# Performance work log

Hardware: AMD Instinct MI355X
Metric: run time of the kernel (lower is better)

Reference implementation:

```python
import jax, jax.numpy as jnp
import numpy as np

B, NPTS = 32, 2048          # batch, raw points per cloud
G, M = 128, 32              # num_group (FPS centers), group_size (KNN)
C, DEPTH, H = 384, 12, 8    # trans_dim, depth, num_heads
HD = C // H                 # head_dim = 48, divisible by 6 for 3-axis RoPE
MLP = 4 * C
CLS = 40
THETA = 100.0


def _ln(x, g, b):
    m = x.mean(-1, keepdims=True)
    v = ((x - m) ** 2).mean(-1, keepdims=True)
    return (x - m) * jax.lax.rsqrt(v + 1e-5) * g + b


def _rot_pairs(x, cos, sin):
    # rotate consecutive (even, odd) pairs of the last dim by angle arrays
    x2 = x.reshape(x.shape[:-1] + (-1, 2))
    xr, xi = x2[..., 0], x2[..., 1]
    return jnp.stack([xr * cos - xi * sin, xr * sin + xi * cos], -1).reshape(x.shape)


def _fps(pts, n):
    # farthest point sampling, first point = index 0
    Bb, N, _ = pts.shape

    def step(carry, _):
        dist, last = carry
        lp = jnp.take_along_axis(pts, last[:, None, None], axis=1)  # (B,1,3)
        dist = jnp.minimum(dist, jnp.sum((pts - lp) ** 2, -1))
        nxt = jnp.argmax(dist, -1).astype(jnp.int32)
        return (dist, nxt), last

    init = (jnp.full((Bb, N), 1e10, pts.dtype), jnp.zeros((Bb,), jnp.int32))
    _, idxs = jax.lax.scan(step, init, None, length=n)
    return idxs.T  # (B, n)


def forward(pts, enc_w1, enc_b1, enc_g1, enc_be1, enc_w2, enc_b2,
            enc_w3, enc_b3, enc_g2, enc_be2, enc_w4, enc_b4,
            cls_token, cls_pos,
            ln1_g, ln1_b, qkv_w, givens_theta, proj_w, proj_b,
            ln2_g, ln2_b, fc1_w, fc1_b, fc2_w, fc2_b,
            norm_g, norm_b,
            hw1, hb1, hg1, hbe1, hw2, hb2, hg2, hbe2, hw3, hb3):
    # ---- Group divider: FPS centers + KNN neighborhoods ----
    cidx = _fps(pts, G)
    center = jnp.take_along_axis(pts, cidx[:, :, None], axis=1)          # (B,G,3)
    d2 = jnp.sum((center[:, :, None, :] - pts[:, None, :, :]) ** 2, -1)  # (B,G,N)
    _, kidx = jax.lax.top_k(-d2, M)                                      # (B,G,M)
    neigh = jax.vmap(lambda p, i: p[i])(pts, kidx) - center[:, :, None, :]

    # ---- mini-PointNet encoder (BN in eval mode: running mean 0, var 1) ----
    x = neigh.reshape(B * G, M, 3)
    f = jax.nn.relu((x @ enc_w1.T + enc_b1) * enc_g1 + enc_be1)          # (BG,M,128)
    f = f @ enc_w2.T + enc_b2                                            # (BG,M,256)
    fg = jnp.max(f, 1, keepdims=True)
    f = jnp.concatenate([jnp.broadcast_to(fg, f.shape), f], -1)          # (BG,M,512)
    f = jax.nn.relu((f @ enc_w3.T + enc_b3) * enc_g2 + enc_be2)
    f = f @ enc_w4.T + enc_b4                                            # (BG,M,C)
    tok = jnp.max(f, 1).reshape(B, G, C)

    # ---- 3-axis axial RoPE frequencies from group centers ----
    nfr = HD // 6
    fr = 1.0 / (THETA ** (jnp.arange(nfr, dtype=pts.dtype) * 2.0 / (HD // 3)))
    ang = (center[..., None] * fr).reshape(B, G, 3 * nfr)                # (B,G,HD/2)
    pcos, psin = jnp.cos(ang)[:, None], jnp.sin(ang)[:, None]            # (B,1,G,HD/2)

    # ---- tokens: [CLS | groups] ----
    x = jnp.concatenate([jnp.broadcast_to(cls_token + cls_pos, (B, 1, C)), tok], 1)
    N = G + 1
    scale = HD ** -0.5

    for i in range(DEPTH):
        h = _ln(x, ln1_g[i], ln1_b[i])
        qkv = (h @ qkv_w[i].T).reshape(B, N, 3, H, HD).transpose(2, 0, 3, 1, 4)
        q, k, v = qkv[0], qkv[1], qkv[2]                                 # (B,H,N,HD)
        # learnable Givens rotation (per-head block-diagonal pair rotations)
        gcos = jnp.cos(givens_theta[i])[None, :, None]                   # (1,H,1,HD/2)
        gsin = jnp.sin(givens_theta[i])[None, :, None]
        q = _rot_pairs(q, gcos, gsin)
        k = _rot_pairs(k, gcos, gsin)
        # positional RoPE on non-CLS tokens only
        q = jnp.concatenate([q[:, :, :1], _rot_pairs(q[:, :, 1:], pcos, psin)], 2)
        k = jnp.concatenate([k[:, :, :1], _rot_pairs(k[:, :, 1:], pcos, psin)], 2)
        attn = jax.nn.softmax(jnp.einsum('bhqd,bhkd->bhqk', q, k) * scale, -1)
        o = jnp.einsum('bhqk,bhkd->bhqd', attn, v).transpose(0, 2, 1, 3).reshape(B, N, C)
        x = x + o @ proj_w[i].T + proj_b[i]
        h = _ln(x, ln2_g[i], ln2_b[i])
        x = x + jax.nn.gelu(h @ fc1_w[i].T + fc1_b[i], approximate=False) @ fc2_w[i].T + fc2_b[i]

    x = _ln(x, norm_g, norm_b)
    feat = jnp.concatenate([x[:, 0], jnp.max(x[:, 1:], 1)], -1)          # (B,2C)
    hfe = jax.nn.relu((feat @ hw1.T + hb1) * hg1 + hbe1)
    hfe = jax.nn.relu((hfe @ hw2.T + hb2) * hg2 + hbe2)
    return hfe @ hw3.T + hb3                                             # (B,CLS)


def setup_inputs() -> dict:
    key = jax.random.key(0)
    ks = iter(jax.random.split(key, 64))
    nrm = lambda *s: jax.random.normal(next(ks), s, jnp.float32) * 0.02
    d = dict(
        pts=jax.random.normal(next(ks), (B, NPTS, 3), jnp.float32),
        enc_w1=nrm(128, 3), enc_b1=jnp.zeros(128), enc_g1=jnp.ones(128), enc_be1=jnp.zeros(128),
        enc_w2=nrm(256, 128), enc_b2=jnp.zeros(256),
        enc_w3=nrm(512, 512), enc_b3=jnp.zeros(512), enc_g2=jnp.ones(512), enc_be2=jnp.zeros(512),
        enc_w4=nrm(C, 512), enc_b4=jnp.zeros(C),
        cls_token=nrm(1, 1, C), cls_pos=nrm(1, 1, C),
        ln1_g=jnp.ones((DEPTH, C)), ln1_b=jnp.zeros((DEPTH, C)),
        qkv_w=nrm(DEPTH, 3 * C, C), givens_theta=nrm(DEPTH, H, HD // 2),
        proj_w=nrm(DEPTH, C, C), proj_b=jnp.zeros((DEPTH, C)),
        ln2_g=jnp.ones((DEPTH, C)), ln2_b=jnp.zeros((DEPTH, C)),
        fc1_w=nrm(DEPTH, MLP, C), fc1_b=jnp.zeros((DEPTH, MLP)),
        fc2_w=nrm(DEPTH, C, MLP), fc2_b=jnp.zeros((DEPTH, C)),
        norm_g=jnp.ones(C), norm_b=jnp.zeros(C),
        hw1=nrm(256, 2 * C), hb1=jnp.zeros(256), hg1=jnp.ones(256), hbe1=jnp.zeros(256),
        hw2=nrm(256, 256), hb2=jnp.zeros(256), hg2=jnp.ones(256), hbe2=jnp.zeros(256),
        hw3=nrm(CLS, 256), hb3=jnp.zeros(CLS),
    )
    return d


def reference(pts, enc_w1, enc_b1, enc_g1, enc_be1, enc_w2, enc_b2,
              enc_w3, enc_b3, enc_g2, enc_be2, enc_w4, enc_b4,
              cls_token, cls_pos,
              ln1_g, ln1_b, qkv_w, givens_theta, proj_w, proj_b,
              ln2_g, ln2_b, fc1_w, fc1_b, fc2_w, fc2_b,
              norm_g, norm_b,
              hw1, hb1, hg1, hbe1, hw2, hb2, hg2, hbe2, hw3, hb3):
    return forward(pts, enc_w1, enc_b1, enc_g1, enc_be1, enc_w2, enc_b2,
                   enc_w3, enc_b3, enc_g2, enc_be2, enc_w4, enc_b4,
                   cls_token, cls_pos,
                   ln1_g, ln1_b, qkv_w, givens_theta, proj_w, proj_b,
                   ln2_g, ln2_b, fc1_w, fc1_b, fc2_w, fc2_b,
                   norm_g, norm_b,
                   hw1, hb1, hg1, hbe1, hw2, hb2, hg2, hbe2, hw3, hb3)
```

## Files before the change

### kernel.cpp

```cpp
#include <hip/hip_runtime.h>
#include <math.h>

constexpr int kB   = 32;
constexpr int kN   = 2048;
constexpr int kG   = 128;
constexpr int kM   = 32;
constexpr int kC   = 384;
constexpr int kH   = 8;
constexpr int kHD  = 48;
constexpr int kNT  = 129;
constexpr int kMLP = 1536;
constexpr int kRows = kB * kNT;
constexpr int kGC  = 512;
constexpr int kRC  = kGC * kM;

typedef __attribute__((ext_vector_type(8))) short bf16x8;
typedef __attribute__((ext_vector_type(4))) float f32x4;

__device__ __forceinline__ unsigned short f2bf(float x) {
  unsigned u = __float_as_uint(x);
  unsigned r = (u + 0x7fffu + ((u >> 16) & 1u)) >> 16;
  return (unsigned short)r;
}
__device__ __forceinline__ float bf2f(unsigned short u) {
  return __uint_as_float(((unsigned)u) << 16);
}

__global__ __launch_bounds__(128, 1) void fps_kernel(
    const float* __restrict__ pts, float* __restrict__ center)
{
  #pragma clang fp contract(off)
  __shared__ float sx[kN + 64], sy[kN + 64], sz[kN + 64];
  __shared__ float rvv[2];
  __shared__ int   rii[2];
  const int b = blockIdx.x, t = threadIdx.x;
  const int lane = t & 63, w = t >> 6;
  const float* P = pts + (size_t)b * kN * 3;
  float rx[16], ry[16], rz[16], rd[16];
  const int base = t * 16;
  #pragma unroll
  for (int j = 0; j < 16; ++j) {
    int i = base + j;
    float x = P[3*i], y = P[3*i+1], z = P[3*i+2];
    rx[j] = x; ry[j] = y; rz[j] = z; rd[j] = 1e10f;
    int ii = i + (i >> 5);
    sx[ii] = x; sy[ii] = y; sz[ii] = z;
  }
  __syncthreads();
  int last = 0;
  float* cb = center + (size_t)b * kG * 3;
  for (int it = 0; it < kG; ++it) {
    int ls = last + (last >> 5);
    float lx = sx[ls], ly = sy[ls], lz = sz[ls];
    if (t == 0) { cb[3*it] = lx; cb[3*it+1] = ly; cb[3*it+2] = lz; }
    float bestv = -1.0f; int besti = kN;
    #pragma unroll
    for (int j = 0; j < 16; ++j) {
      float dx = rx[j]-lx, dy = ry[j]-ly, dz = rz[j]-lz;
      float d = (dx*dx + dy*dy) + dz*dz;
      float nd = fminf(rd[j], d);
      rd[j] = nd;
      if (nd > bestv) { bestv = nd; besti = base + j; }
    }
    #pragma unroll
    for (int off = 1; off < 64; off <<= 1) {
      float vv = __shfl_xor(bestv, off);
      int   ii = __shfl_xor(besti, off);
      if (vv > bestv || (vv == bestv && ii < besti)) { bestv = vv; besti = ii; }
    }
    if (lane == 0) { rvv[w] = bestv; rii[w] = besti; }
    __syncthreads();
    float v0 = rvv[0], v1 = rvv[1];
    int   i0 = rii[0], i1 = rii[1];
    last = (v1 > v0) ? i1 : i0;
    __syncthreads();
  }
}

__global__ void rope_kernel(const float* __restrict__ center,
                            float* __restrict__ pcs, float* __restrict__ psn)
{
  int idx = blockIdx.x*256 + threadIdx.x;
  if (idx >= kB*kG*24) return;
  int p  = idx % 24;
  int bg = idx / 24;
  int axis = p >> 3, j = p & 7;
  float e  = (float)(2*j) / 16.0f;
  float fr = 1.0f / powf(100.0f, e);
  float ang = center[(size_t)bg*3 + axis] * fr;
  pcs[idx] = cosf(ang);
  psn[idx] = sinf(ang);
}

__global__ __launch_bounds__(256) void knn_kernel(
    const float* __restrict__ pts, const float* __restrict__ center,
    float* __restrict__ neigh)
{
  #pragma clang fp contract(off)
  __shared__ float sx[kN + kN/32], sy[kN + kN/32], sz[kN + kN/32];
  const int t = threadIdx.x;
  const int lane = t & 63, w = t >> 6;
  const int blk = blockIdx.x;
  const int b = blk >> 5;
  const float* P = pts + (size_t)b * kN * 3;
  for (int i = t; i < kN; i += 256) {
    int ii = i + (i >> 5);
    sx[ii] = P[3*i]; sy[ii] = P[3*i+1]; sz[ii] = P[3*i+2];
  }
  __syncthreads();
  const int bg = b*kG + (blk & 31)*4 + w;
  const float cx = center[(size_t)bg*3+0];
  const float cy = center[(size_t)bg*3+1];
  const float cz = center[(size_t)bg*3+2];
  float rd[32];
  const int base = lane * 32;
  #pragma unroll
  for (int j = 0; j < 32; ++j) {
    int is = lane*33 + j;
    float dx = cx - sx[is], dy = cy - sy[is], dz = cz - sz[is];
    rd[j] = (dx*dx + dy*dy) + dz*dz;
  }
  float* ob = neigh + (size_t)bg * kM * 3;
  int lastWin = -1;
  for (int m = 0; m < kM; ++m) {
    float bestv = 3.0e38f; int besti = kN;
    #pragma unroll
    for (int j = 0; j < 32; ++j) {
      float v = rd[j];
      if (base + j == lastWin) v = 3.0e38f;
      rd[j] = v;
      if (v < bestv) { bestv = v; besti = base + j; }
    }
    #pragma unroll
    for (int off = 1; off < 64; off <<= 1) {
      float vv = __shfl_xor(bestv, off);
      int   i2 = __shfl_xor(besti, off);
      if (vv < bestv || (vv == bestv && i2 < besti)) { bestv = vv; besti = i2; }
    }
    lastWin = besti;
    if (lane == 0) {
      int is = besti + (besti >> 5);
      ob[3*m+0] = sx[is] - cx; ob[3*m+1] = sy[is] - cy; ob[3*m+2] = sz[is] - cz;
    }
  }
}

__global__ void wcvt_kernel(const float* __restrict__ s,
                            unsigned short* __restrict__ d, int n)
{
  int i = (blockIdx.x*256 + threadIdx.x)*8;
  if (i >= n) return;
  float4 a = *(const float4*)(s + i), b = *(const float4*)(s + i + 4);
  bf16x8 v;
  v[0]=(short)f2bf(a.x); v[1]=(short)f2bf(a.y); v[2]=(short)f2bf(a.z); v[3]=(short)f2bf(a.w);
  v[4]=(short)f2bf(b.x); v[5]=(short)f2bf(b.y); v[6]=(short)f2bf(b.z); v[7]=(short)f2bf(b.w);
  *(bf16x8*)(d + i) = v;
}

__global__ void wcvt4_kernel(const float* __restrict__ q, const float* __restrict__ p,
                             const float* __restrict__ f1, const float* __restrict__ f2,
                             unsigned short* __restrict__ d)
{
  int i = (blockIdx.x*256 + threadIdx.x)*8;
  const float* s; int lo;
  if (i < 442368)       { s = q;  lo = i; }
  else if (i < 589824)  { s = p;  lo = i - 442368; }
  else if (i < 1179648) { s = f1; lo = i - 589824; }
  else                  { s = f2; lo = i - 1179648; }
  float4 a = *(const float4*)(s + lo), b = *(const float4*)(s + lo + 4);
  bf16x8 v;
  v[0]=(short)f2bf(a.x); v[1]=(short)f2bf(a.y); v[2]=(short)f2bf(a.z); v[3]=(short)f2bf(a.w);
  v[4]=(short)f2bf(b.x); v[5]=(short)f2bf(b.y); v[6]=(short)f2bf(b.z); v[7]=(short)f2bf(b.w);
  *(bf16x8*)(d + i) = v;
}

__global__ __launch_bounds__(256) void enc1_kernel(
    const float* __restrict__ neighC,
    const float* __restrict__ w1, const float* __restrict__ b1,
    const float* __restrict__ g1, const float* __restrict__ be1,
    unsigned short* __restrict__ f1c)
{
  const int t = threadIdx.x;
  const int r = blockIdx.x*2 + (t >> 7);
  const int c = t & 127;
  const float* nr = neighC + (size_t)r*3;
  float x0 = nr[0], x1 = nr[1], x2 = nr[2];
  float s = x0*w1[3*c] + x1*w1[3*c+1] + x2*w1[3*c+2] + b1[c];
  float v = fmaxf(s*g1[c] + be1[c], 0.0f);
  f1c[(size_t)r*128 + c] = f2bf(v);
}

__global__ __launch_bounds__(256) void pool2_kernel(
    const unsigned short* __restrict__ f2c, unsigned short* __restrict__ fgc)
{
  const int g = blockIdx.x, c = threadIdx.x;
  float mx = -3.0e38f;
  #pragma unroll 8
  for (int m = 0; m < kM; ++m)
    mx = fmaxf(mx, bf2f(f2c[((size_t)g*kM + m)*256 + c]));
  fgc[(size_t)g*256 + c] = f2bf(mx);
}

template <int EPI, int FM, int FN>
__global__ __launch_bounds__(256) void mgemm_kernel(
    const unsigned short* __restrict__ A, int lda,
    const unsigned short* __restrict__ Bb, int ldb,
    void* __restrict__ Cv,
    const float* __restrict__ bias,
    const float* __restrict__ aux,
    const float* __restrict__ gsc, const float* __restrict__ bsc,
    int Mm, int Nn, int Kk,
    float* __restrict__ poolOut, int poolG0)
{
  constexpr int BM = FM*32, BN = FN*32;
  __shared__ unsigned short As[BM][72];
  __shared__ unsigned short Bs[BN][72];
  const int t = threadIdx.x;
  const int m0 = blockIdx.x * BM;
  const int n0 = blockIdx.y * BN;
  const int w = t >> 6, lane = t & 63;
  const int wm = w >> 1, wn = w & 1;
  const int lr = lane & 15;
  const int lk = (lane >> 4) * 8;
  const int srow = t >> 3;
  const int skseg = (t & 7) * 8;
  f32x4 acc[FM][FN] = {};
  for (int k0 = 0; k0 < Kk; k0 += 64) {
    #pragma unroll
    for (int p = 0; p < BM/32; ++p) {
      int r = p*32 + srow;
      int gr = m0 + r;
      bf16x8 av = {};
      if (gr < Mm) av = *(const bf16x8*)(A + (size_t)gr*lda + k0 + skseg);
      *(bf16x8*)(&As[r][skseg]) = av;
    }
    #pragma unroll
    for (int p = 0; p < BN/32; ++p) {
      int r = p*32 + srow;
      bf16x8 bv = *(const bf16x8*)(Bb + (size_t)(n0 + r)*ldb + k0 + skseg);
      *(bf16x8*)(&Bs[r][skseg]) = bv;
    }
    __syncthreads();
    #pragma unroll
    for (int kk = 0; kk < 64; kk += 32) {
      bf16x8 af[FM], bf[FN];
      #pragma unroll
      for (int i = 0; i < FM; ++i)
        af[i] = *(const bf16x8*)(&As[wm*(FM*16) + i*16 + lr][kk + lk]);
      #pragma unroll
      for (int i = 0; i < FN; ++i)
        bf[i] = *(const bf16x8*)(&Bs[wn*(FN*16) + i*16 + lr][kk + lk]);
      #pragma unroll
      for (int i = 0; i < FM; ++i)
        #pragma unroll
        for (int j = 0; j < FN; ++j)
          acc[i][j] = __builtin_amdgcn_mfma_f32_16x16x32_bf16(af[i], bf[j], acc[i][j], 0, 0, 0);
    }
    __syncthreads();
  }

  if constexpr (EPI == 4) {
    #pragma unroll
    for (int ni = 0; ni < FN; ++ni) {
      int cc = n0 + wn*(FN*16) + ni*16 + lr;
      float mx = -3.0e38f;
      #pragma unroll
      for (int mi = 0; mi < FM; ++mi)
        #pragma unroll
        for (int j = 0; j < 4; ++j)
          mx = fmaxf(mx, acc[mi][ni][j]);
      mx = fmaxf(mx, __shfl_xor(mx, 16));
      mx = fmaxf(mx, __shfl_xor(mx, 32));
      if ((lane >> 4) == 0) {
        int ggl = poolG0 + (m0 >> 5) + wm;
        int b = ggl >> 7, g = ggl & 127;
        poolOut[((size_t)b*kNT + 1 + g)*kC + cc] = mx + bias[cc];
      }
    }
    return;
  }

  #pragma unroll
  for (int mi = 0; mi < FM; ++mi) {
    #pragma unroll
    for (int j = 0; j < 4; ++j) {
      int r = m0 + wm*(FM*16) + mi*16 + (lane >> 4)*4 + j;
      if (r < Mm) {
        #pragma unroll
        for (int ni = 0; ni < FN; ++ni) {
          int cc = n0 + wn*(FN*16) + ni*16 + lr;
          float v = acc[mi][ni][j];
          size_t o = (size_t)r*Nn + cc;
          if constexpr (EPI == 0) {
            ((unsigned short*)Cv)[o] = f2bf(v);
          } else if constexpr (EPI == 1) {
            ((unsigned short*)Cv)[o] = f2bf(v + bias[cc]);
          } else if constexpr (EPI == 2) {
            ((float*)Cv)[o] = v + bias[cc];
          } else if constexpr (EPI == 3) {
            float u = (v + aux[(size_t)(r >> 5)*Nn + cc])*gsc[cc] + bsc[cc];
            ((unsigned short*)Cv)[o] = f2bf(fmaxf(u, 0.0f));
          } else if constexpr (EPI == 5) {
            ((float*)Cv)[o] = aux[o] + v + bias[cc];
          } else {
            float u = v + bias[cc];
            ((unsigned short*)Cv)[o] = f2bf(0.5f*u*(1.0f + erff(u*0.70710678118654752440f)));
          }
        }
      }
    }
  }
}

__global__ void cls_kernel(const float* __restrict__ ct, const float* __restrict__ cp,
                           float* __restrict__ x)
{
  int idx = blockIdx.x*256 + threadIdx.x;
  if (idx >= kB*kC) return;
  int b = idx / kC, c = idx % kC;
  x[(size_t)b*kNT*kC + c] = ct[c] + cp[c];
}

template <int OUTBF>
__global__ __launch_bounds__(256) void ln_kernel(
    const float* __restrict__ in, void* __restrict__ outv,
    const float* __restrict__ g, const float* __restrict__ bb)
{
  const int t = threadIdx.x;
  const int lane = t & 63;
  const int row = blockIdx.x*4 + (t >> 6);
  const float* p = in + (size_t)row*kC;
  float v[6];
  #pragma unroll
  for (int k = 0; k < 6; ++k) v[k] = p[k*64 + lane];
  float s = 0.f;
  #pragma unroll
  for (int k = 0; k < 6; ++k) s += v[k];
  #pragma unroll
  for (int off = 1; off < 64; off <<= 1) s += __shfl_xor(s, off);
  float mean = s / 384.0f;
  float vs = 0.f;
  #pragma unroll
  for (int k = 0; k < 6; ++k) { float d = v[k]-mean; vs += d*d; }
  #pragma unroll
  for (int off = 1; off < 64; off <<= 1) vs += __shfl_xor(vs, off);
  float r = rsqrtf(vs / 384.0f + 1e-5f);
  #pragma unroll
  for (int k = 0; k < 6; ++k) {
    int c = k*64 + lane;
    float o = (v[k]-mean)*r*g[c] + bb[c];
    if constexpr (OUTBF) ((unsigned short*)outv)[(size_t)row*kC + c] = f2bf(o);
    else                 ((float*)outv)[(size_t)row*kC + c] = o;
  }
}

__global__ __launch_bounds__(512) void attn_kernel(
    const unsigned short* __restrict__ qkv, const float* __restrict__ pcs,
    const float* __restrict__ psn, const float* __restrict__ gth,
    unsigned short* __restrict__ o)
{
  __shared__ float qs[kNT][kHD];
  __shared__ float ks[kNT][52];
  __shared__ float vt[kHD][132];
  __shared__ float gcs[24], gss[24];
  __shared__ float ps[8][132];
  const int t = threadIdx.x;
  const int bh = blockIdx.x;
  const int b = bh >> 3, hh = bh & 7;
  if (t < 24) { float th = gth[hh*24 + t]; gcs[t] = cosf(th); gss[t] = sinf(th); }
  __syncthreads();
  for (int idx = t; idx < kNT*24; idx += 512) {
    int n = idx / 24, p = idx % 24;
    const unsigned short* base = qkv + ((size_t)(b*kNT + n))*1152 + hh*kHD + 2*p;
    float q0 = bf2f(base[0]),   q1 = bf2f(base[1]);
    float k0 = bf2f(base[384]), k1 = bf2f(base[385]);
    float v0 = bf2f(base[768]), v1 = bf2f(base[769]);
    float cg = gcs[p], sg = gss[p];
    float qr = q0*cg - q1*sg, qi = q0*sg + q1*cg;
    float kr = k0*cg - k1*sg, ki = k0*sg + k1*cg;
    if (n > 0) {
      size_t pi = ((size_t)b*kG + (n-1))*24 + p;
      float pc = pcs[pi], pv = psn[pi];
      float tq = qr*pc - qi*pv; qi = qr*pv + qi*pc; qr = tq;
      float tk = kr*pc - ki*pv; ki = kr*pv + ki*pc; kr = tk;
    }
    qs[n][2*p] = qr; qs[n][2*p+1] = qi;
    ks[n][2*p] = kr; ks[n][2*p+1] = ki;
    vt[2*p][n] = v0; vt[2*p+1][n] = v1;
  }
  __syncthreads();
  const int lane = t & 63, w = t >> 6;
  for (int r = w; r < kNT; r += 8) {
    float4 q[12];
    #pragma unroll
    for (int d = 0; d < 12; ++d) q[d] = *(const float4*)(&qs[r][d*4]);
    float sv[3];
    float mx = -3.0e38f;
    #pragma unroll
    for (int ji = 0; ji < 3; ++ji) {
      int j = ji*64 + lane;
      float s = -3.0e38f;
      if (j < kNT) {
        float a0 = 0.f, a1 = 0.f;
        #pragma unroll
        for (int d = 0; d < 12; d += 2) {
          float4 k0v = *(const float4*)(&ks[j][d*4]);
          float4 k1v = *(const float4*)(&ks[j][d*4+4]);
          a0 += q[d].x*k0v.x + q[d].y*k0v.y + q[d].z*k0v.z + q[d].w*k0v.w;
          a1 += q[d+1].x*k1v.x + q[d+1].y*k1v.y + q[d+1].z*k1v.z + q[d+1].w*k1v.w;
        }
        s = (a0 + a1) * 0.14433756729740643f;
      }
      sv[ji] = s;
      mx = fmaxf(mx, s);
    }
    #pragma unroll
    for (int off = 1; off < 64; off <<= 1) mx = fmaxf(mx, __shfl_xor(mx, off));
    float sum = 0.f;
    #pragma unroll
    for (int ji = 0; ji < 3; ++ji) {
      int j = ji*64 + lane;
      if (j < kNT) { float e = expf(sv[ji] - mx); ps[w][j] = e; sum += e; }
    }
    #pragma unroll
    for (int off = 1; off < 64; off <<= 1) sum += __shfl_xor(sum, off);
    if (lane < kHD) {
      float ac0 = 0.f, ac1 = 0.f, ac2 = 0.f, ac3 = 0.f;
      for (int j4 = 0; j4 < 128; j4 += 16) {
        float4 p0 = *(const float4*)(&ps[w][j4]);
        float4 p1 = *(const float4*)(&ps[w][j4+4]);
        float4 p2 = *(const float4*)(&ps[w][j4+8]);
        float4 p3 = *(const float4*)(&ps[w][j4+12]);
        float4 v0 = *(const float4*)(&vt[lane][j4]);
        float4 v1 = *(const float4*)(&vt[lane][j4+4]);
        float4 v2 = *(const float4*)(&vt[lane][j4+8]);
        float4 v3 = *(const float4*)(&vt[lane][j4+12]);
        ac0 += p0.x*v0.x + p0.y*v0.y + p0.z*v0.z + p0.w*v0.w;
        ac1 += p1.x*v1.x + p1.y*v1.y + p1.z*v1.z + p1.w*v1.w;
        ac2 += p2.x*v2.x + p2.y*v2.y + p2.z*v2.z + p2.w*v2.w;
        ac3 += p3.x*v3.x + p3.y*v3.y + p3.z*v3.z + p3.w*v3.w;
      }
      float accv = ((ac0 + ac1) + (ac2 + ac3)) + ps[w][128]*vt[lane][128];
      o[((size_t)(b*kNT + r))*kC + hh*kHD + lane] = f2bf(accv / sum);
    }
  }
}

__global__ __launch_bounds__(256) void head_kernel(
    const float* __restrict__ xf,
    const float* __restrict__ hw1, const float* __restrict__ hb1,
    const float* __restrict__ hg1, const float* __restrict__ hbe1,
    const float* __restrict__ hw2, const float* __restrict__ hb2,
    const float* __restrict__ hg2, const float* __restrict__ hbe2,
    const float* __restrict__ hw3, const float* __restrict__ hb3,
    float* __restrict__ out)
{
  __shared__ float f[768];
  __shared__ float h1[256], h2[256];
  const int t = threadIdx.x;
  const int b = blockIdx.x;
  const float* xb = xf + (size_t)b*kNT*kC;
  for (int c = t; c < kC; c += 256) {
    f[c] = xb[c];
    float mx = -3.0e38f;
    for (int n = 1; n < kNT; ++n) mx = fmaxf(mx, xb[(size_t)n*kC + c]);
    f[kC + c] = mx;
  }
  __syncthreads();
  {
    float acc = hb1[t];
    for (int k = 0; k < 768; k += 4) {
      float4 wv = *(const float4*)(hw1 + (size_t)t*768 + k);
      float4 fv = *(const float4*)(&f[k]);
      acc += fv.x*wv.x + fv.y*wv.y + fv.z*wv.z + fv.w*wv.w;
    }
    h1[t] = fmaxf(acc*hg1[t] + hbe1[t], 0.0f);
  }
  __syncthreads();
  {
    float acc = hb2[t];
    for (int k = 0; k < 256; k += 4) {
      float4 wv = *(const float4*)(hw2 + (size_t)t*256 + k);
      float4 fv = *(const float4*)(&h1[k]);
      acc += fv.x*wv.x + fv.y*wv.y + fv.z*wv.z + fv.w*wv.w;
    }
    h2[t] = fmaxf(acc*hg2[t] + hbe2[t], 0.0f);
  }
  __syncthreads();
  if (t < 40) {
    float acc = hb3[t];
    for (int k = 0; k < 256; k += 4) {
      float4 wv = *(const float4*)(hw3 + (size_t)t*256 + k);
      float4 fv = *(const float4*)(&h2[k]);
      acc += fv.x*wv.x + fv.y*wv.y + fv.z*wv.z + fv.w*wv.w;
    }
    out[(size_t)b*40 + t] = acc;
  }
}

extern "C" void kernel_launch(void* const* d_in, const int* in_sizes, int n_in,
                              void* d_out, int out_size, void* d_ws, size_t ws_size,
                              hipStream_t stream) {
  const float* pts     = (const float*)d_in[0];
  const float* enc_w1  = (const float*)d_in[1];
  const float* enc_b1  = (const float*)d_in[2];
  const float* enc_g1  = (const float*)d_in[3];
  const float* enc_be1 = (const float*)d_in[4];
  const float* enc_w2  = (const float*)d_in[5];
  const float* enc_b2  = (const float*)d_in[6];
  const float* enc_w3  = (const float*)d_in[7];
  const float* enc_b3  = (const float*)d_in[8];
  const float* enc_g2  = (const float*)d_in[9];
  const float* enc_be2 = (const float*)d_in[10];
  const float* enc_w4  = (const float*)d_in[11];
  const float* enc_b4  = (const float*)d_in[12];
  const float* cls_tok = (const float*)d_in[13];
  const float* cls_pos = (const float*)d_in[14];
  const float* ln1_g   = (const float*)d_in[15];
  const float* ln1_b   = (const float*)d_in[16];
  const float* qkv_w   = (const float*)d_in[17];
  const float* givens  = (const float*)d_in[18];
  const float* proj_w  = (const float*)d_in[19];
  const float* proj_b  = (const float*)d_in[20];
  const float* ln2_g   = (const float*)d_in[21];
  const float* ln2_b   = (const float*)d_in[22];
  const float* fc1_w   = (const float*)d_in[23];
  const float* fc1_b   = (const float*)d_in[24];
  const float* fc2_w   = (const float*)d_in[25];
  const float* fc2_b   = (const float*)d_in[26];
  const float* norm_g  = (const float*)d_in[27];
  const float* norm_b  = (const float*)d_in[28];
  const float* hw1     = (const float*)d_in[29];
  const float* hb1     = (const float*)d_in[30];
  const float* hg1     = (const float*)d_in[31];
  const float* hbe1    = (const float*)d_in[32];
  const float* hw2     = (const float*)d_in[33];
  const float* hb2     = (const float*)d_in[34];
  const float* hg2     = (const float*)d_in[35];
  const float* hbe2    = (const float*)d_in[36];
  const float* hw3     = (const float*)d_in[37];
  const float* hb3     = (const float*)d_in[38];

  constexpr size_t kWL = 1769472ull;
  char* wsb = (char*)d_ws;
  size_t off = 0;
  float* center = (float*)(wsb + off); off += (size_t)kB*kG*3*4;
  float* pcs    = (float*)(wsb + off); off += (size_t)kB*kG*24*4;
  float* psn    = (float*)(wsb + off); off += (size_t)kB*kG*24*4;
  float* neigh  = (float*)(wsb + off); off += (size_t)kB*kG*kM*3*4;
  float* xbuf   = (float*)(wsb + off); off += (size_t)kRows*kC*4;
  unsigned short* encwb = (unsigned short*)(wsb + off); off += 491520ull*2;
  unsigned short* wlbf  = (unsigned short*)(wsb + off);
  const size_t scratchNeed = 16777216ull + 8388608ull + 262144ull + 1048576ull;
  const bool bigws = ws_size >= off + 12*kWL*2 + scratchNeed;
  off += (bigws ? 12*kWL*2 : kWL*2);
  char* scratch = wsb + off;
  unsigned short* f3c   = (unsigned short*)(scratch);
  unsigned short* f1c   = (unsigned short*)(scratch);
  unsigned short* f2c   = (unsigned short*)(scratch + 16777216);
  unsigned short* fgc   = (unsigned short*)(scratch + 16777216 + 8388608);
  float*          basec = (float*)(scratch + 16777216 + 8388608 + 262144);
  unsigned short* hbuf   = (unsigned short*)(scratch);
  unsigned short* qkvb   = (unsigned short*)(scratch + 3170304);
  unsigned short* attnob = (unsigned short*)(scratch + 3170304 + 9510912);
  unsigned short* mlpb   = (unsigned short*)(scratch + 3170304);
  float*          flnb   = (float*)(scratch + 3170304);

  const unsigned short* encw2 = encwb;
  const unsigned short* encw3 = encwb + 32768;
  const unsigned short* encw4 = encwb + 32768 + 262144;

  fps_kernel<<<kB, 128, 0, stream>>>(pts, center);
  rope_kernel<<<(kB*kG*24 + 255)/256, 256, 0, stream>>>(center, pcs, psn);
  knn_kernel<<<kB*kG/4, 256, 0, stream>>>(pts, center, neigh);

  wcvt_kernel<<<32768/8/256, 256, 0, stream>>>(enc_w2, (unsigned short*)encw2, 32768);
  wcvt_kernel<<<262144/8/256, 256, 0, stream>>>(enc_w3, (unsigned short*)encw3, 262144);
  wcvt_kernel<<<196608/8/256, 256, 0, stream>>>(enc_w4, (unsigned short*)encw4, 196608);
  if (bigws) {
    for (int l = 0; l < 12; ++l)
      wcvt4_kernel<<<864, 256, 0, stream>>>(
          qkv_w + (size_t)l*442368, proj_w + (size_t)l*147456,
          fc1_w + (size_t)l*589824, fc2_w + (size_t)l*589824, wlbf + (size_t)l*kWL);
  }

  for (int c = 0; c < 8; ++c) {
    const float* nc = neigh + (size_t)c*kRC*3;
    enc1_kernel<<<kRC/2, 256, 0, stream>>>(nc, enc_w1, enc_b1, enc_g1, enc_be1, f1c);
    mgemm_kernel<1,2,2><<<dim3(kRC/64, 4), 256, 0, stream>>>(
        f1c, 128, encw2, 128, f2c, enc_b2, nullptr, nullptr, nullptr,
        kRC, 256, 128, nullptr, 0);
    pool2_kernel<<<kGC, 256, 0, stream>>>(f2c, fgc);
    mgemm_kernel<2,2,2><<<dim3(kGC/64, 8), 256, 0, stream>>>(
        fgc, 256, encw3, 512, basec, enc_b3, nullptr, nullptr, nullptr,
        kGC, 512, 256, nullptr, 0);
    mgemm_kernel<3,2,2><<<dim3(kRC/64, 8), 256, 0, stream>>>(
        f2c, 256, encw3 + 256, 512, f3c, nullptr, basec, enc_g2, enc_be2,
        kRC, 512, 256, nullptr, 0);
    mgemm_kernel<4,2,2><<<dim3(kRC/64, 6), 256, 0, stream>>>(
        f3c, 512, encw4, 512, nullptr, enc_b4, nullptr, nullptr, nullptr,
        kRC, 384, 512, xbuf, c*kGC);
  }
  cls_kernel<<<(kB*kC + 255)/256, 256, 0, stream>>>(cls_tok, cls_pos, xbuf);

  const int lnGrid = kRows/4;
  for (int l = 0; l < 12; ++l) {
    unsigned short* wl = wlbf + (bigws ? (size_t)l*kWL : 0);
    if (!bigws)
      wcvt4_kernel<<<864, 256, 0, stream>>>(
          qkv_w + (size_t)l*442368, proj_w + (size_t)l*147456,
          fc1_w + (size_t)l*589824, fc2_w + (size_t)l*589824, wl);
    const unsigned short* wq  = wl;
    const unsigned short* wp  = wl + 442368;
    const unsigned short* w1f = wl + 589824;
    const unsigned short* w2f = wl + 1179648;
    ln_kernel<1><<<lnGrid, 256, 0, stream>>>(xbuf, hbuf, ln1_g + l*kC, ln1_b + l*kC);
    mgemm_kernel<0,2,2><<<dim3(65, 18), 256, 0, stream>>>(
        hbuf, kC, wq, kC, qkvb, nullptr, nullptr, nullptr, nullptr,
        kRows, 1152, kC, nullptr, 0);
    attn_kernel<<<kB*kH, 512, 0, stream>>>(qkvb, pcs, psn, givens + (size_t)l*kH*24, attnob);
    mgemm_kernel<5,2,2><<<dim3(65, 6), 256, 0, stream>>>(
        attnob, kC, wp, kC, xbuf, proj_b + l*kC, xbuf, nullptr, nullptr,
        kRows, kC, kC, nullptr, 0);
    ln_kernel<1><<<lnGrid, 256, 0, stream>>>(xbuf, hbuf, ln2_g + l*kC, ln2_b + l*kC);
    mgemm_kernel<6,2,2><<<dim3(65, 24), 256, 0, stream>>>(
        hbuf, kC, w1f, kC, mlpb, fc1_b + l*kMLP, nullptr, nullptr, nullptr,
        kRows, kMLP, kC, nullptr, 0);
    mgemm_kernel<5,2,2><<<dim3(65, 6), 256, 0, stream>>>(
        mlpb, kMLP, w2f, kMLP, xbuf, fc2_b + l*kC, xbuf, nullptr, nullptr,
        kRows, kC, kMLP, nullptr, 0);
  }
  ln_kernel<0><<<lnGrid, 256, 0, stream>>>(xbuf, flnb, norm_g, norm_b);
  head_kernel<<<kB, 256, 0, stream>>>(flnb,
      hw1, hb1, hg1, hbe1, hw2, hb2, hg2, hbe2, hw3, hb3, (float*)d_out);
}
```

Baseline: 2.348 ms.

## Load GEMM B tiles directly to LDS with pre-swizzled bf16 weights

The weight conversion kernels now write bf16 weights with an XOR swizzle on 8-element chunks within each 64-wide K block. The GEMM stages its B tile into LDS with global_load_lds, skipping the register round-trip, and the swizzle gives conflict-free fragment reads without padding. Separately, the FPS kernel stops holding point coordinates in registers and reads a float4 array from LDS on every iteration. That lowers register pressure but adds LDS traffic inside the serial FPS loop. Any other GEMM whose B operand is not produced by these conversion kernels would now read it with the wrong layout.

```diff
diff --git a/kernel.cpp b/kernel.cpp
--- a/kernel.cpp
+++ b/kernel.cpp
@@ -26,37 +26,43 @@
   return __uint_as_float(((unsigned)u) << 16);
 }
 
+__device__ __forceinline__ void gld_lds16(const void* g, void* l) {
+  __builtin_amdgcn_global_load_lds(
+      (const __attribute__((address_space(1))) unsigned int*)g,
+      (__attribute__((address_space(3))) unsigned int*)l, 16, 0, 0);
+}
+
 __global__ __launch_bounds__(128, 1) void fps_kernel(
     const float* __restrict__ pts, float* __restrict__ center)
 {
   #pragma clang fp contract(off)
-  __shared__ float sx[kN + 64], sy[kN + 64], sz[kN + 64];
+  __shared__ float4 s4[kN + kN/32 + 1];
   __shared__ float rvv[2];
   __shared__ int   rii[2];
   const int b = blockIdx.x, t = threadIdx.x;
   const int lane = t & 63, w = t >> 6;
   const float* P = pts + (size_t)b * kN * 3;
-  float rx[16], ry[16], rz[16], rd[16];
-  const int base = t * 16;
+  float rd[16];
+  const int base  = t * 16;
+  const int gbase = t * 16 + (t >> 1);
   #pragma unroll
   for (int j = 0; j < 16; ++j) {
     int i = base + j;
-    float x = P[3*i], y = P[3*i+1], z = P[3*i+2];
-    rx[j] = x; ry[j] = y; rz[j] = z; rd[j] = 1e10f;
-    int ii = i + (i >> 5);
-    sx[ii] = x; sy[ii] = y; sz[ii] = z;
+    s4[gbase + j] = make_float4(P[3*i], P[3*i+1], P[3*i+2], 0.0f);
+    rd[j] = 1e10f;
   }
   __syncthreads();
   int last = 0;
   float* cb = center + (size_t)b * kG * 3;
   for (int it = 0; it < kG; ++it) {
     int ls = last + (last >> 5);
-    float lx = sx[ls], ly = sy[ls], lz = sz[ls];
-    if (t == 0) { cb[3*it] = lx; cb[3*it+1] = ly; cb[3*it+2] = lz; }
+    float4 L = s4[ls];
+    if (t == 0) { cb[3*it] = L.x; cb[3*it+1] = L.y; cb[3*it+2] = L.z; }
     float bestv = -1.0f; int besti = kN;
     #pragma unroll
     for (int j = 0; j < 16; ++j) {
-      float dx = rx[j]-lx, dy = ry[j]-ly, dz = rz[j]-lz;
+      float4 p = s4[gbase + j];
+      float dx = p.x - L.x, dy = p.y - L.y, dz = p.z - L.z;
       float d = (dx*dx + dy*dy) + dz*dz;
       float nd = fminf(rd[j], d);
       rd[j] = nd;
@@ -146,15 +152,17 @@
 }
 
 __global__ void wcvt_kernel(const float* __restrict__ s,
-                            unsigned short* __restrict__ d, int n)
+                            unsigned short* __restrict__ d, int n, int K)
 {
   int i = (blockIdx.x*256 + threadIdx.x)*8;
   if (i >= n) return;
+  int row = i / K, k = i % K;
+  int dk = (k & ~63) | (((((k >> 3) & 7)) ^ (row & 7)) << 3);
   float4 a = *(const float4*)(s + i), b = *(const float4*)(s + i + 4);
   bf16x8 v;
   v[0]=(short)f2bf(a.x); v[1]=(short)f2bf(a.y); v[2]=(short)f2bf(a.z); v[3]=(short)f2bf(a.w);
   v[4]=(short)f2bf(b.x); v[5]=(short)f2bf(b.y); v[6]=(short)f2bf(b.z); v[7]=(short)f2bf(b.w);
-  *(bf16x8*)(d + i) = v;
+  *(bf16x8*)(d + (size_t)row*K + dk) = v;
 }
 
 __global__ void wcvt4_kernel(const float* __restrict__ q, const float* __restrict__ p,
@@ -162,16 +170,18 @@
                              unsigned short* __restrict__ d)
 {
   int i = (blockIdx.x*256 + threadIdx.x)*8;
-  const float* s; int lo;
-  if (i < 442368)       { s = q;  lo = i; }
-  else if (i < 589824)  { s = p;  lo = i - 442368; }
-  else if (i < 1179648) { s = f1; lo = i - 589824; }
-  else                  { s = f2; lo = i - 1179648; }
+  const float* s; int lo, K;
+  if (i < 442368)       { s = q;  lo = i;           K = 384; }
+  else if (i < 589824)  { s = p;  lo = i - 442368;  K = 384; }
+  else if (i < 1179648) { s = f1; lo = i - 589824;  K = 384; }
+  else                  { s = f2; lo = i - 1179648; K = 1536; }
+  int row = lo / K, k = lo % K;
+  int dk = (k & ~63) | (((((k >> 3) & 7)) ^ (row & 7)) << 3);
   float4 a = *(const float4*)(s + lo), b = *(const float4*)(s + lo + 4);
   bf16x8 v;
   v[0]=(short)f2bf(a.x); v[1]=(short)f2bf(a.y); v[2]=(short)f2bf(a.z); v[3]=(short)f2bf(a.w);
   v[4]=(short)f2bf(b.x); v[5]=(short)f2bf(b.y); v[6]=(short)f2bf(b.z); v[7]=(short)f2bf(b.w);
-  *(bf16x8*)(d + i) = v;
+  *(bf16x8*)(d + (size_t)(i - lo) + (size_t)row*K + dk) = v;
 }
 
 __global__ __launch_bounds__(256) void enc1_kernel(
@@ -214,7 +224,7 @@
 {
   constexpr int BM = FM*32, BN = FN*32;
   __shared__ unsigned short As[BM][72];
-  __shared__ unsigned short Bs[BN][72];
+  __shared__ unsigned short BsL[BN*64];
   const int t = threadIdx.x;
   const int m0 = blockIdx.x * BM;
   const int n0 = blockIdx.y * BN;
@@ -222,8 +232,11 @@
   const int wm = w >> 1, wn = w & 1;
   const int lr = lane & 15;
   const int lk = (lane >> 4) * 8;
+  const int lx7 = lr & 7;
   const int srow = t >> 3;
   const int skseg = (t & 7) * 8;
+  const int brow = lane >> 3;
+  const int bm8  = (lane & 7) * 8;
   f32x4 acc[FM][FN] = {};
   for (int k0 = 0; k0 < Kk; k0 += 64) {
     #pragma unroll
@@ -235,10 +248,10 @@
       *(bf16x8*)(&As[r][skseg]) = av;
     }
     #pragma unroll
-    for (int p = 0; p < BN/32; ++p) {
-      int r = p*32 + srow;
-      bf16x8 bv = *(const bf16x8*)(Bb + (size_t)(n0 + r)*ldb + k0 + skseg);
-      *(bf16x8*)(&Bs[r][skseg]) = bv;
+    for (int c = 0; c < BN/32; ++c) {
+      int q = w*(BN/32) + c;
+      int r = q*8 + brow;
+      gld_lds16(Bb + (size_t)(n0 + r)*ldb + k0 + bm8, BsL + q*512);
     }
     __syncthreads();
     #pragma unroll
@@ -248,8 +261,11 @@
       for (int i = 0; i < FM; ++i)
         af[i] = *(const bf16x8*)(&As[wm*(FM*16) + i*16 + lr][kk + lk]);
       #pragma unroll
-      for (int i = 0; i < FN; ++i)
-        bf[i] = *(const bf16x8*)(&Bs[wn*(FN*16) + i*16 + lr][kk + lk]);
+      for (int i = 0; i < FN; ++i) {
+        int rr = wn*(FN*16) + i*16 + lr;
+        int c8 = (kk + lk) >> 3;
+        bf[i] = *(const bf16x8*)(&BsL[rr*64 + ((c8 ^ lx7) << 3)]);
+      }
       #pragma unroll
       for (int i = 0; i < FM; ++i)
         #pragma unroll
@@ -574,9 +590,9 @@
   rope_kernel<<<(kB*kG*24 + 255)/256, 256, 0, stream>>>(center, pcs, psn);
   knn_kernel<<<kB*kG/4, 256, 0, stream>>>(pts, center, neigh);
 
-  wcvt_kernel<<<32768/8/256, 256, 0, stream>>>(enc_w2, (unsigned short*)encw2, 32768);
-  wcvt_kernel<<<262144/8/256, 256, 0, stream>>>(enc_w3, (unsigned short*)encw3, 262144);
-  wcvt_kernel<<<196608/8/256, 256, 0, stream>>>(enc_w4, (unsigned short*)encw4, 196608);
+  wcvt_kernel<<<32768/8/256, 256, 0, stream>>>(enc_w2, (unsigned short*)encw2, 32768, 128);
+  wcvt_kernel<<<262144/8/256, 256, 0, stream>>>(enc_w3, (unsigned short*)encw3, 262144, 512);
+  wcvt_kernel<<<196608/8/256, 256, 0, stream>>>(enc_w4, (unsigned short*)encw4, 196608, 512);
   if (bigws) {
     for (int l = 0; l < 12; ++l)
       wcvt4_kernel<<<864, 256, 0, stream>>>(
```

New measurement: 2.481 ms. 5.6% more time.
